# Kernel tuning notes

Measured on AMD Instinct MI355X. Metric: run time of the kernel, lower is better.

The kernel has to match this reference:

```python
import jax, jax.numpy as jnp
import numpy as np

D_EMBED = 512
NUM_HEADS = 8
HEAD_DIM = D_EMBED // NUM_HEADS
D_FF = 2048
B, L = 2, 4096
LN_EPS = 1e-5


def _layernorm(x, g, b):
    mu = jnp.mean(x, axis=-1, keepdims=True)
    var = jnp.mean(jnp.square(x - mu), axis=-1, keepdims=True)
    return (x - mu) * jax.lax.rsqrt(var + LN_EPS) * g + b


def setup_inputs() -> dict:
    key = jax.random.key(0)
    ks = jax.random.split(key, 16)
    s = 0.02
    inp = {
        "x": jax.random.normal(ks[0], (B, L, D_EMBED), dtype=jnp.float32),
        "mask": jnp.ones((B, 1, 1, L), dtype=jnp.int32),
        # attention projections (stored [in, out] for x @ W)
        "Wq": jax.random.normal(ks[1], (D_EMBED, D_EMBED), dtype=jnp.float32) * s,
        "bq": jnp.zeros((D_EMBED,), dtype=jnp.float32),
        "Wk": jax.random.normal(ks[2], (D_EMBED, D_EMBED), dtype=jnp.float32) * s,
        "bk": jnp.zeros((D_EMBED,), dtype=jnp.float32),
        "Wv": jax.random.normal(ks[3], (D_EMBED, D_EMBED), dtype=jnp.float32) * s,
        "bv": jnp.zeros((D_EMBED,), dtype=jnp.float32),
        "Wo": jax.random.normal(ks[4], (D_EMBED, D_EMBED), dtype=jnp.float32) * s,
        "bo": jnp.zeros((D_EMBED,), dtype=jnp.float32),
        # layernorms
        "ln1_g": jnp.ones((D_EMBED,), dtype=jnp.float32),
        "ln1_b": jnp.zeros((D_EMBED,), dtype=jnp.float32),
        "ln2_g": jnp.ones((D_EMBED,), dtype=jnp.float32),
        "ln2_b": jnp.zeros((D_EMBED,), dtype=jnp.float32),
        # FFN
        "W1": jax.random.normal(ks[5], (D_EMBED, D_FF), dtype=jnp.float32) * s,
        "b1": jnp.zeros((D_FF,), dtype=jnp.float32),
        "W2": jax.random.normal(ks[6], (D_FF, D_EMBED), dtype=jnp.float32) * s,
        "b2": jnp.zeros((D_EMBED,), dtype=jnp.float32),
    }
    return inp


def reference(x, mask, Wq, bq, Wk, bk, Wv, bv, Wo, bo, ln1_g, ln1_b,
              W1, b1, W2, b2, ln2_g, ln2_b):
    Bx, Lx, _ = x.shape
    # projections -> [B, H, L, Dh]
    def split_heads(t):
        return t.reshape(Bx, Lx, NUM_HEADS, HEAD_DIM).transpose(0, 2, 1, 3)
    q = split_heads(x @ Wq + bq)
    k = split_heads(x @ Wk + bk)
    v = split_heads(x @ Wv + bv)
    scores = jnp.einsum("bhqd,bhkd->bhqk", q, k) / jnp.sqrt(
        jnp.asarray(HEAD_DIM, dtype=x.dtype))
    scores = jnp.where(mask == 0, jnp.asarray(-1e9, dtype=x.dtype), scores)
    attn = jax.nn.softmax(scores, axis=-1)
    ctx = jnp.einsum("bhqk,bhkd->bhqd", attn, v)
    ctx = ctx.transpose(0, 2, 1, 3).reshape(Bx, Lx, D_EMBED)
    attn_out = ctx @ Wo + bo

    h = _layernorm(x + attn_out, ln1_g, ln1_b)
    ff = (jax.nn.gelu(h @ W1 + b1, approximate=False)) @ W2 + b2
    return _layernorm(h + ff, ln2_g, ln2_b)
```

## Files before the change

kernel.cpp:

```cpp
#include <hip/hip_runtime.h>
#include <hip/hip_bf16.h>
#include <math.h>

#define D_EMBED 512
#define NUM_HEADS 8
#define HEAD_DIM 64
#define D_FF 2048
#define BATCH 2
#define SEQ 4096
#define M_ROWS (BATCH*SEQ)
#define QSCALE 0.18033688011112042f

typedef __attribute__((ext_vector_type(8))) short short8;
typedef __attribute__((ext_vector_type(4))) short short4_t;
typedef __attribute__((ext_vector_type(4))) float f32x4;

#if __has_builtin(__builtin_amdgcn_mfma_f32_16x16x16bf16_1k)
#define MFMA_K16(a,b,c) __builtin_amdgcn_mfma_f32_16x16x16bf16_1k(a,b,c,0,0,0)
#elif __has_builtin(__builtin_amdgcn_mfma_f32_16x16x16_bf16)
#define MFMA_K16(a,b,c) __builtin_amdgcn_mfma_f32_16x16x16_bf16(a,b,c,0,0,0)
#else
#define MFMA_K16(a,b,c) (c)
#endif

#if __has_builtin(__builtin_amdgcn_exp2f)
#define EXP2(x) __builtin_amdgcn_exp2f(x)
#else
#define EXP2(x) exp2f(x)
#endif

__device__ inline unsigned short f2b(float f) {
    union { float f; unsigned u; } v; v.f = f;
    unsigned r = v.u + 0x7fffu + ((v.u >> 16) & 1u);
    return (unsigned short)(r >> 16);
}

__device__ inline float b2f(short s) {
    union { unsigned u; float f; } v;
    v.u = ((unsigned)(unsigned short)s) << 16;
    return v.f;
}

__device__ inline short4_t pk4(float p0, float p1, float p2, float p3) {
    union { __hip_bfloat162 h2[2]; short4_t s4; } u;
    u.h2[0] = __float22bfloat162_rn(make_float2(p0, p1));
    u.h2[1] = __float22bfloat162_rn(make_float2(p2, p3));
    return u.s4;
}

__device__ inline void gl2lds16(const void* g, void* l) {
    __builtin_amdgcn_global_load_lds(
        (const __attribute__((address_space(1))) unsigned int*)g,
        (__attribute__((address_space(3))) unsigned int*)l, 16, 0, 0);
}

template<int EPI>
__global__ __launch_bounds__(256) void gemm_bt(
    const unsigned short* __restrict__ A, const unsigned short* __restrict__ BT,
    const float* __restrict__ bias, void* __restrict__ Cout,
    int M, int N, int K)
{
    __shared__ __align__(16) unsigned short As[128*32];
    __shared__ __align__(16) unsigned short Bs[128*32];
    const int tid  = threadIdx.x;
    const int wave = tid >> 6, lane = tid & 63;
    const int wy = wave >> 1, wx = wave & 1;
    const int quad = lane >> 4, m16 = lane & 15;
    const int row0 = blockIdx.y * 128, n0 = blockIdx.x * 128;
    const int rdoff = (quad ^ ((m16 >> 1) & 3)) * 8;

    f32x4 acc[4][4];
#pragma unroll
    for (int i = 0; i < 4; i++)
#pragma unroll
        for (int j = 0; j < 4; j++) acc[i][j] = (f32x4){0.f,0.f,0.f,0.f};

    const int kIters = K >> 5;
    for (int kt = 0; kt < kIters; ++kt) {
        const int k0 = kt << 5;
#pragma unroll
        for (int it = 0; it < 2; ++it) {
            int g  = it*256 + tid;
            int r  = g >> 2;
            int c8 = (((g & 3) ^ ((g >> 3) & 3)) << 3);
            gl2lds16(A  + (size_t)(row0 + r)*K + k0 + c8, &As[(size_t)(it*256 + wave*64)*8]);
            gl2lds16(BT + (size_t)(n0  + r)*K + k0 + c8, &Bs[(size_t)(it*256 + wave*64)*8]);
        }
        __syncthreads();
        short8 a[4], b[4];
#pragma unroll
        for (int i = 0; i < 4; i++) a[i] = *(const short8*)&As[(wy*64 + i*16 + m16)*32 + rdoff];
#pragma unroll
        for (int j = 0; j < 4; j++) b[j] = *(const short8*)&Bs[(wx*64 + j*16 + m16)*32 + rdoff];
#pragma unroll
        for (int i = 0; i < 4; i++)
#pragma unroll
            for (int j = 0; j < 4; j++)
                acc[i][j] = __builtin_amdgcn_mfma_f32_16x16x32_bf16(a[i], b[j], acc[i][j], 0, 0, 0);
        __syncthreads();
    }

#pragma unroll
    for (int j = 0; j < 4; j++) {
        int col = n0 + wx*64 + j*16 + m16;
        float bj = bias[col];
#pragma unroll
        for (int i = 0; i < 4; i++) {
            int rbase = row0 + wy*64 + i*16 + quad*4;
#pragma unroll
            for (int r = 0; r < 4; r++) {
                float v = acc[i][j][r] + bj;
                size_t idx = (size_t)(rbase + r)*N + col;
                if (EPI == 0) {
                    ((unsigned short*)Cout)[idx] = f2b(v);
                } else {
                    float gv = 0.5f * v * (1.0f + erff(v * 0.70710678118654752f));
                    ((unsigned short*)Cout)[idx] = f2b(gv);
                }
            }
        }
    }
}

__global__ __launch_bounds__(256) void gemm_qkv(
    const unsigned short* __restrict__ A, const unsigned short* __restrict__ BT,
    const float* __restrict__ bias,
    unsigned short* __restrict__ Qp, unsigned short* __restrict__ Kp,
    unsigned short* __restrict__ Vp)
{
    const int K = 512;
    __shared__ __align__(16) unsigned short As[128*32];
    __shared__ __align__(16) unsigned short Bs[128*32];
    const int tid  = threadIdx.x;
    const int wave = tid >> 6, lane = tid & 63;
    const int wy = wave >> 1, wx = wave & 1;
    const int quad = lane >> 4, m16 = lane & 15;
    const int row0 = blockIdx.y * 128, n0 = blockIdx.x * 128;
    const int rdoff = (quad ^ ((m16 >> 1) & 3)) * 8;
    const int region = n0 >> 9;

    f32x4 acc[4][4];
#pragma unroll
    for (int i = 0; i < 4; i++)
#pragma unroll
        for (int j = 0; j < 4; j++) acc[i][j] = (f32x4){0.f,0.f,0.f,0.f};

    for (int kt = 0; kt < 16; ++kt) {
        const int k0 = kt << 5;
#pragma unroll
        for (int it = 0; it < 2; ++it) {
            int g  = it*256 + tid;
            int r  = g >> 2;
            int c8 = (((g & 3) ^ ((g >> 3) & 3)) << 3);
            gl2lds16(A  + (size_t)(row0 + r)*K + k0 + c8, &As[(size_t)(it*256 + wave*64)*8]);
            gl2lds16(BT + (size_t)(n0  + r)*K + k0 + c8, &Bs[(size_t)(it*256 + wave*64)*8]);
        }
        __syncthreads();
        short8 a[4], b[4];
#pragma unroll
        for (int i = 0; i < 4; i++) a[i] = *(const short8*)&As[(wy*64 + i*16 + m16)*32 + rdoff];
#pragma unroll
        for (int j = 0; j < 4; j++) b[j] = *(const short8*)&Bs[(wx*64 + j*16 + m16)*32 + rdoff];
#pragma unroll
        for (int i = 0; i < 4; i++)
#pragma unroll
            for (int j = 0; j < 4; j++)
                acc[i][j] = __builtin_amdgcn_mfma_f32_16x16x32_bf16(a[i], b[j], acc[i][j], 0, 0, 0);
        __syncthreads();
    }

    const float sc = (region == 0) ? QSCALE : 1.0f;
#pragma unroll
    for (int j = 0; j < 4; j++) {
        int col = n0 + wx*64 + j*16 + m16;
        float bj = bias[col];
        int cc = col & 511, h = cc >> 6, d = cc & 63;
#pragma unroll
        for (int i = 0; i < 4; i++) {
            int rbase = row0 + wy*64 + i*16 + quad*4;
#pragma unroll
            for (int r = 0; r < 4; r++) {
                float v = (acc[i][j][r] + bj) * sc;
                int row = rbase + r;
                int b = row >> 12, l = row & 4095;
                size_t bh = (size_t)(b*8 + h);
                if (region == 0) {
                    Qp[(bh*SEQ + l)*64 + d] = f2b(v);
                } else if (region == 1) {
                    Kp[(bh*SEQ + l)*64 + d] = f2b(v);
                } else {
                    int kt = l >> 7, kk = l & 127;
                    int qr = (kk >> 2) & 3, fi = (kk >> 4)*4 + (kk & 3);
                    Vp[((((bh*32 + kt)*4 + qr)*64 + d)*32) + fi] = f2b(v);
                }
            }
        }
    }
}

__global__ __launch_bounds__(256) void gemm_bt64(
    const unsigned short* __restrict__ A, const unsigned short* __restrict__ BT,
    const float* __restrict__ bias, unsigned short* __restrict__ Cout,
    int M, int N, int K)
{
    __shared__ __align__(16) unsigned short As[64*32];
    __shared__ __align__(16) unsigned short Bs[128*32];
    const int tid  = threadIdx.x;
    const int wave = tid >> 6, lane = tid & 63;
    const int wy = wave >> 1, wx = wave & 1;
    const int quad = lane >> 4, m16 = lane & 15;
    const int row0 = blockIdx.y * 64, n0 = blockIdx.x * 128;
    const int rdoff = (quad ^ ((m16 >> 1) & 3)) * 8;

    f32x4 acc[2][4];
#pragma unroll
    for (int i = 0; i < 2; i++)
#pragma unroll
        for (int j = 0; j < 4; j++) acc[i][j] = (f32x4){0.f,0.f,0.f,0.f};

    const int kIters = K >> 5;
    for (int kt = 0; kt < kIters; ++kt) {
        const int k0 = kt << 5;
        {
            int r = tid >> 2;
            int c8 = (((tid & 3) ^ ((tid >> 3) & 3)) << 3);
            gl2lds16(A + (size_t)(row0 + r)*K + k0 + c8, &As[(size_t)(wave*64)*8]);
        }
#pragma unroll
        for (int it = 0; it < 2; ++it) {
            int g  = it*256 + tid;
            int r  = g >> 2;
            int c8 = (((g & 3) ^ ((g >> 3) & 3)) << 3);
            gl2lds16(BT + (size_t)(n0 + r)*K + k0 + c8, &Bs[(size_t)(it*256 + wave*64)*8]);
        }
        __syncthreads();
        short8 a[2], b[4];
#pragma unroll
        for (int i = 0; i < 2; i++) a[i] = *(const short8*)&As[(wy*32 + i*16 + m16)*32 + rdoff];
#pragma unroll
        for (int j = 0; j < 4; j++) b[j] = *(const short8*)&Bs[(wx*64 + j*16 + m16)*32 + rdoff];
#pragma unroll
        for (int i = 0; i < 2; i++)
#pragma unroll
            for (int j = 0; j < 4; j++)
                acc[i][j] = __builtin_amdgcn_mfma_f32_16x16x32_bf16(a[i], b[j], acc[i][j], 0, 0, 0);
        __syncthreads();
    }

#pragma unroll
    for (int j = 0; j < 4; j++) {
        int col = n0 + wx*64 + j*16 + m16;
        float bj = bias[col];
#pragma unroll
        for (int i = 0; i < 2; i++) {
            int rbase = row0 + wy*32 + i*16 + quad*4;
#pragma unroll
            for (int r = 0; r < 4; r++) {
                float v = acc[i][j][r] + bj;
                Cout[(size_t)(rbase + r)*N + col] = f2b(v);
            }
        }
    }
}

__global__ __launch_bounds__(256) void prep(
    const float* __restrict__ Wq, const float* __restrict__ Wk,
    const float* __restrict__ Wv, const float* __restrict__ Wo,
    const float* __restrict__ W1, const float* __restrict__ W2,
    const float* __restrict__ bq, const float* __restrict__ bk,
    const float* __restrict__ bv, const int* __restrict__ mask,
    unsigned short* __restrict__ WqkvT, unsigned short* __restrict__ WoT,
    unsigned short* __restrict__ W1T, unsigned short* __restrict__ W2T,
    float* __restrict__ bqkv, int* __restrict__ mflag, unsigned* __restrict__ kmax2)
{
    const int id = blockIdx.x, t = threadIdx.x;
    if (id == 3072) {
        if (t < 64) {
            const int* m = mask + t*128;
            int all = 1;
            for (int i = 0; i < 128; i += 4) {
                int4 v = *(const int4*)(m + i);
                all &= (v.x && v.y && v.z && v.w) ? 1 : 0;
            }
            mflag[t] = all;
        }
        if (t < 16) kmax2[t] = 0u;
        for (int i = t; i < 1536; i += 256)
            bqkv[i] = (i < 512) ? bq[i] : ((i < 1024) ? bk[i-512] : bv[i-1024]);
        return;
    }
    __shared__ float tt[32][33];
    const float* W; unsigned short* WT; int K, N, bx, by;
    if (id < 256)       { W = Wq; WT = WqkvT;            K = 512;  N = 512;  bx = id & 15;  by = id >> 4; }
    else if (id < 512)  { int l = id - 256;  W = Wk; WT = WqkvT + 512*512;  K = 512;  N = 512;  bx = l & 15; by = l >> 4; }
    else if (id < 768)  { int l = id - 512;  W = Wv; WT = WqkvT + 1024*512; K = 512;  N = 512;  bx = l & 15; by = l >> 4; }
    else if (id < 1024) { int l = id - 768;  W = Wo; WT = WoT;              K = 512;  N = 512;  bx = l & 15; by = l >> 4; }
    else if (id < 2048) { int l = id - 1024; W = W1; WT = W1T;              K = 512;  N = 2048; bx = l & 63; by = l >> 6; }
    else                { int l = id - 2048; W = W2; WT = W2T;              K = 2048; N = 512;  bx = l & 15; by = l >> 4; }
    const int n0 = bx*32, k0 = by*32;
    const int x = t & 31, y = t >> 5;
#pragma unroll
    for (int yy = y; yy < 32; yy += 8) tt[yy][x] = W[(size_t)(k0+yy)*N + n0 + x];
    __syncthreads();
#pragma unroll
    for (int yy = y; yy < 32; yy += 8) WT[(size_t)(n0+yy)*K + k0 + x] = f2b(tt[x][yy]);
}

__global__ __launch_bounds__(256) void kmax_k(
    const unsigned short* __restrict__ Kp, unsigned* __restrict__ kmax2)
{
    const int bh = blockIdx.x, t = threadIdx.x;
    const int row = blockIdx.y*256 + t;
    const unsigned short* kp = Kp + ((size_t)bh*SEQ + row)*64;
    float s = 0.f;
#pragma unroll
    for (int c = 0; c < 8; ++c) {
        short8 v = *(const short8*)(kp + c*8);
#pragma unroll
        for (int j = 0; j < 8; ++j) { float f = b2f(v[j]); s += f*f; }
    }
#pragma unroll
    for (int off = 32; off >= 1; off >>= 1)
        s = fmaxf(s, __shfl_xor(s, off, 64));
    if ((t & 63) == 0) atomicMax(&kmax2[bh], __float_as_uint(s));
}

__global__ __launch_bounds__(256) void flash_attn(
    const unsigned short* __restrict__ Qp, const unsigned short* __restrict__ Kp,
    const unsigned short* __restrict__ Vp, const int* __restrict__ mask,
    const int* __restrict__ flags, const unsigned* __restrict__ kmax2,
    unsigned short* __restrict__ O)
{
    __shared__ __align__(16) unsigned short Ks[2][128*32];
    __shared__ __align__(16) unsigned short Vs[4][64*32];
    const int tid = threadIdx.x, wave = tid >> 6, lane = tid & 63;
    const int quad = lane >> 4, m16 = lane & 15;
    const int bh = blockIdx.y, b = bh >> 3, h = bh & 7;
    const int qbase = blockIdx.x * 64 + wave * 16;
    const int fsw = (m16 >> 1) & 3;
    const int koff = (quad ^ fsw) * 8;

    const unsigned short* Qb = Qp + (size_t)bh*SEQ*64;
    const unsigned short* Kb = Kp + (size_t)bh*SEQ*64;
    const unsigned short* Vb = Vp + (size_t)bh*32*4*64*32;
    const int* mbase = mask + b*SEQ;
    const int* fbase = flags + b*(SEQ/128);

    short8 qf[2];
    {
        const unsigned short* qp = Qb + (size_t)(qbase + m16)*64 + quad*8;
        qf[0] = *(const short8*)qp;
        qf[1] = *(const short8*)(qp + 32);
    }
    float qn2 = 0.f;
#pragma unroll
    for (int j = 0; j < 8; ++j) {
        float f0 = b2f(qf[0][j]), f1 = b2f(qf[1][j]);
        qn2 += f0*f0 + f1*f1;
    }
    qn2 += __shfl_xor(qn2, 16, 64);
    qn2 += __shfl_xor(qn2, 32, 64);
    const float M = sqrtf(qn2 * __uint_as_float(kmax2[bh]));
    const f32x4 cinit = (f32x4){-M, -M, -M, -M};

    f32x4 accO[4];
#pragma unroll
    for (int dj = 0; dj < 4; dj++) accO[dj] = (f32x4){0.f,0.f,0.f,0.f};
    float rs = 0.f;

    for (int kt = 0; kt < SEQ/128; ++kt) {
        const int key0 = kt * 128;
        const int allones = fbase[kt];
        __syncthreads();
#pragma unroll
        for (int it = 0; it < 2; ++it) {
            int g = it*256 + tid;
            int r = g >> 2;
            int c8 = (((g & 3) ^ ((g >> 3) & 3)) << 3);
            gl2lds16(Kb + (size_t)(key0 + r)*64 + c8,      &Ks[0][(it*256 + wave*64)*8]);
            gl2lds16(Kb + (size_t)(key0 + r)*64 + 32 + c8, &Ks[1][(it*256 + wave*64)*8]);
        }
        {
            int d = wave*16 + (lane >> 2), ch = lane & 3;
            int c8 = (ch ^ ((d >> 1) & 3)) * 8;
#pragma unroll
            for (int qr = 0; qr < 4; ++qr)
                gl2lds16(Vb + (((size_t)kt*4 + qr)*64 + d)*32 + c8,
                         &Vs[qr][wave*64*8]);
        }
        __syncthreads();

        short4_t pb[8];
#pragma unroll
        for (int nj = 0; nj < 8; ++nj) {
            short8 k0 = *(const short8*)&Ks[0][(nj*16 + m16)*32 + koff];
            short8 k1 = *(const short8*)&Ks[1][(nj*16 + m16)*32 + koff];
            f32x4 c = cinit;
            c = __builtin_amdgcn_mfma_f32_16x16x32_bf16(k0, qf[0], c, 0, 0, 0);
            c = __builtin_amdgcn_mfma_f32_16x16x32_bf16(k1, qf[1], c, 0, 0, 0);
            if (!allones) {
                int4 mv = *(const int4*)(mbase + key0 + nj*16 + quad*4);
                c[0] = mv.x ? c[0] : -1e9f;
                c[1] = mv.y ? c[1] : -1e9f;
                c[2] = mv.z ? c[2] : -1e9f;
                c[3] = mv.w ? c[3] : -1e9f;
            }
            float p0 = EXP2(c[0]);
            float p1 = EXP2(c[1]);
            float p2 = EXP2(c[2]);
            float p3 = EXP2(c[3]);
            rs += (p0 + p1) + (p2 + p3);
            pb[nj] = pk4(p0, p1, p2, p3);
        }

#pragma unroll
        for (int l = 0; l < 4; ++l) {
#pragma unroll
            for (int dj = 0; dj < 4; ++dj) {
                const unsigned short* vrow = &Vs[quad][(dj*16 + m16)*32 + ((l ^ fsw) * 8)];
                short4_t vlo = *(const short4_t*)vrow;
                short4_t vhi = *(const short4_t*)(vrow + 4);
                accO[dj] = MFMA_K16(vlo, pb[2*l],     accO[dj]);
                accO[dj] = MFMA_K16(vhi, pb[2*l + 1], accO[dj]);
            }
        }
    }

    rs += __shfl_xor(rs, 16, 64);
    rs += __shfl_xor(rs, 32, 64);
    float rl = 1.0f / rs;
#pragma unroll
    for (int dj = 0; dj < 4; ++dj) {
        short4_t o = pk4(accO[dj][0]*rl, accO[dj][1]*rl,
                         accO[dj][2]*rl, accO[dj][3]*rl);
        *(short4_t*)&O[(size_t)(b*SEQ + qbase + m16)*D_EMBED
                       + h*HEAD_DIM + dj*16 + quad*4] = o;
    }
}

__global__ __launch_bounds__(256) void ln_res1(
    const float* __restrict__ A, const unsigned short* __restrict__ Bv,
    const float* __restrict__ g, const float* __restrict__ be,
    unsigned short* __restrict__ Yb)
{
    const int wave = threadIdx.x >> 6, lane = threadIdx.x & 63;
    const int row = blockIdx.x * 4 + wave;
    const float* ap = A + (size_t)row*512 + lane*8;
    short8 bv = *(const short8*)(Bv + (size_t)row*512 + lane*8);
    float v[8]; float s = 0.f;
#pragma unroll
    for (int j = 0; j < 8; j++) { v[j] = ap[j] + b2f(bv[j]); s += v[j]; }
#pragma unroll
    for (int off = 32; off >= 1; off >>= 1) s += __shfl_xor(s, off, 64);
    float mu = s * (1.f/512.f);
    float q = 0.f;
#pragma unroll
    for (int j = 0; j < 8; j++) { v[j] -= mu; q += v[j]*v[j]; }
#pragma unroll
    for (int off = 32; off >= 1; off >>= 1) q += __shfl_xor(q, off, 64);
    float rstd = rsqrtf(q * (1.f/512.f) + 1e-5f);
#pragma unroll
    for (int j = 0; j < 8; j++) {
        float y = v[j]*rstd*g[lane*8+j] + be[lane*8+j];
        Yb[(size_t)row*512 + lane*8 + j] = f2b(y);
    }
}

__global__ __launch_bounds__(256) void ln_res2(
    const unsigned short* __restrict__ A, const unsigned short* __restrict__ Bv,
    const float* __restrict__ g, const float* __restrict__ be,
    float* __restrict__ Yf)
{
    const int wave = threadIdx.x >> 6, lane = threadIdx.x & 63;
    const int row = blockIdx.x * 4 + wave;
    short8 av = *(const short8*)(A  + (size_t)row*512 + lane*8);
    short8 bv = *(const short8*)(Bv + (size_t)row*512 + lane*8);
    float v[8]; float s = 0.f;
#pragma unroll
    for (int j = 0; j < 8; j++) { v[j] = b2f(av[j]) + b2f(bv[j]); s += v[j]; }
#pragma unroll
    for (int off = 32; off >= 1; off >>= 1) s += __shfl_xor(s, off, 64);
    float mu = s * (1.f/512.f);
    float q = 0.f;
#pragma unroll
    for (int j = 0; j < 8; j++) { v[j] -= mu; q += v[j]*v[j]; }
#pragma unroll
    for (int off = 32; off >= 1; off >>= 1) q += __shfl_xor(q, off, 64);
    float rstd = rsqrtf(q * (1.f/512.f) + 1e-5f);
#pragma unroll
    for (int j = 0; j < 8; j++) {
        float y = v[j]*rstd*g[lane*8+j] + be[lane*8+j];
        Yf[(size_t)row*512 + lane*8 + j] = y;
    }
}

__global__ __launch_bounds__(256) void cvt_f32_bf16(
    const float* __restrict__ X, unsigned short* __restrict__ Y, int n)
{
    int idx = (blockIdx.x * 256 + threadIdx.x) * 4;
    if (idx < n) {
        float4 v = *(const float4*)(X + idx);
        Y[idx+0] = f2b(v.x); Y[idx+1] = f2b(v.y);
        Y[idx+2] = f2b(v.z); Y[idx+3] = f2b(v.w);
    }
}

extern "C" void kernel_launch(void* const* d_in, const int* in_sizes, int n_in,
                              void* d_out, int out_size, void* d_ws, size_t ws_size,
                              hipStream_t stream)
{
    const float* x    = (const float*)d_in[0];
    const int*   mask = (const int*)  d_in[1];
    const float* Wq = (const float*)d_in[2];  const float* bq = (const float*)d_in[3];
    const float* Wk = (const float*)d_in[4];  const float* bk = (const float*)d_in[5];
    const float* Wv = (const float*)d_in[6];  const float* bv = (const float*)d_in[7];
    const float* Wo = (const float*)d_in[8];  const float* bo = (const float*)d_in[9];
    const float* ln1g = (const float*)d_in[10]; const float* ln1b = (const float*)d_in[11];
    const float* ln2g = (const float*)d_in[12]; const float* ln2b = (const float*)d_in[13];
    const float* W1 = (const float*)d_in[14]; const float* b1 = (const float*)d_in[15];
    const float* W2 = (const float*)d_in[16]; const float* b2 = (const float*)d_in[17];
    float* out = (float*)d_out;

    char* ws = (char*)d_ws;
    const size_t MB = 1024*1024;
    unsigned short* xb    = (unsigned short*)(ws + 0);
    unsigned short* WqkvT = (unsigned short*)(ws + 8*MB);
    unsigned short* W1T   = (unsigned short*)(ws + 10*MB);
    unsigned short* W2T   = (unsigned short*)(ws + 12*MB);
    unsigned short* WoT   = (unsigned short*)(ws + 14*MB);
    float*          bqkv  = (float*)(ws + 14*MB + 512*1024);
    int*            mflag = (int*)(ws + 14*MB + 768*1024);
    unsigned*       kmaxb = (unsigned*)(ws + 14*MB + 772*1024);
    unsigned short* Qp    = (unsigned short*)(ws + 15*MB);
    unsigned short* Kp    = (unsigned short*)(ws + 23*MB);
    unsigned short* Vp    = (unsigned short*)(ws + 31*MB);
    unsigned short* ctx   = (unsigned short*)(ws + 39*MB);
    unsigned short* atfb  = (unsigned short*)(ws + 47*MB);
    unsigned short* hb    = (unsigned short*)(ws + 0);
    unsigned short* Gb    = (unsigned short*)(ws + 15*MB);
    unsigned short* ffb   = (unsigned short*)(ws + 47*MB);

    cvt_f32_bf16<<<4096, 256, 0, stream>>>(x, xb, M_ROWS*D_EMBED);
    prep<<<3073, 256, 0, stream>>>(Wq, Wk, Wv, Wo, W1, W2, bq, bk, bv, mask,
                                   WqkvT, WoT, W1T, W2T, bqkv, mflag, kmaxb);

    gemm_qkv<<<dim3(12,64), 256, 0, stream>>>(xb, WqkvT, bqkv, Qp, Kp, Vp);

    kmax_k<<<dim3(16,16), 256, 0, stream>>>(Kp, kmaxb);
    flash_attn<<<dim3(SEQ/64, 16), 256, 0, stream>>>(Qp, Kp, Vp, mask, mflag, kmaxb, ctx);

    gemm_bt64<<<dim3(4,128), 256, 0, stream>>>(ctx, WoT, bo, atfb, M_ROWS, 512, 512);
    ln_res1<<<M_ROWS/4, 256, 0, stream>>>(x, atfb, ln1g, ln1b, hb);

    gemm_bt<2><<<dim3(16,64), 256, 0, stream>>>(hb, W1T, b1, Gb, M_ROWS, D_FF, 512);
    gemm_bt64<<<dim3(4,128), 256, 0, stream>>>(Gb, W2T, b2, ffb, M_ROWS, 512, D_FF);
    ln_res2<<<M_ROWS/4, 256, 0, stream>>>(hb, ffb, ln2g, ln2b, out);
}
```

Baseline: 377.1 us.

## Rewrite flash attention with 32x32 MFMA, 64 queries per wave, double-buffered K/V

The attention kernel now handles 64 queries per wave (256 per block) using 32x32x16 bf16 MFMA tiles, so each K/V tile loaded into LDS is reused across four times as many queries. K and V tiles for the next 128-key step are prefetched into a second LDS buffer while the current one is computed, which removes one barrier per iteration. V is now stored transposed as [bh][d][seq], and the P fragments are rearranged in registers with permlane32 swaps. The cost is a grid of only 256 blocks with a heavier register footprint, which can hurt occupancy and leave some CUs underused.

```diff
diff --git a/kernel.cpp b/kernel.cpp
--- a/kernel.cpp
+++ b/kernel.cpp
@@ -14,14 +14,7 @@
 typedef __attribute__((ext_vector_type(8))) short short8;
 typedef __attribute__((ext_vector_type(4))) short short4_t;
 typedef __attribute__((ext_vector_type(4))) float f32x4;
-
-#if __has_builtin(__builtin_amdgcn_mfma_f32_16x16x16bf16_1k)
-#define MFMA_K16(a,b,c) __builtin_amdgcn_mfma_f32_16x16x16bf16_1k(a,b,c,0,0,0)
-#elif __has_builtin(__builtin_amdgcn_mfma_f32_16x16x16_bf16)
-#define MFMA_K16(a,b,c) __builtin_amdgcn_mfma_f32_16x16x16_bf16(a,b,c,0,0,0)
-#else
-#define MFMA_K16(a,b,c) (c)
-#endif
+typedef __attribute__((ext_vector_type(16))) float f32x16;
 
 #if __has_builtin(__builtin_amdgcn_exp2f)
 #define EXP2(x) __builtin_amdgcn_exp2f(x)
@@ -46,6 +39,36 @@
     u.h2[0] = __float22bfloat162_rn(make_float2(p0, p1));
     u.h2[1] = __float22bfloat162_rn(make_float2(p2, p3));
     return u.s4;
+}
+
+__device__ inline unsigned pk2(float lo, float hi) {
+    union { __hip_bfloat162 h2; unsigned u; } x;
+    x.h2 = __float22bfloat162_rn(make_float2(lo, hi));
+    return x.u;
+}
+
+__device__ inline void plswap(unsigned a, unsigned b, unsigned &r0, unsigned &r1) {
+#if __has_builtin(__builtin_amdgcn_permlane32_swap)
+    auto v = __builtin_amdgcn_permlane32_swap(a, b, false, false);
+    r0 = (unsigned)v[0]; r1 = (unsigned)v[1];
+#else
+    unsigned ax = (unsigned)__shfl_xor((int)a, 32, 64);
+    unsigned bx = (unsigned)__shfl_xor((int)b, 32, 64);
+    bool hi = (threadIdx.x & 32) != 0;
+    r0 = hi ? bx : a;
+    r1 = hi ? b  : ax;
+#endif
+}
+
+__device__ inline short8 pfrag8(const float* p) {
+    unsigned a0 = pk2(p[0], p[1]), a1 = pk2(p[2], p[3]);
+    unsigned b0 = pk2(p[4], p[5]), b1 = pk2(p[6], p[7]);
+    unsigned u0, u1, u2, u3;
+    plswap(a0, b0, u0, u1);
+    plswap(a1, b1, u2, u3);
+    union { unsigned u[4]; short8 s; } r;
+    r.u[0] = u0; r.u[1] = u2; r.u[2] = u1; r.u[3] = u3;
+    return r.s;
 }
 
 __device__ inline void gl2lds16(const void* g, void* l) {
@@ -189,9 +212,7 @@
                 } else if (region == 1) {
                     Kp[(bh*SEQ + l)*64 + d] = f2b(v);
                 } else {
-                    int kt = l >> 7, kk = l & 127;
-                    int qr = (kk >> 2) & 3, fi = (kk >> 4)*4 + (kk & 3);
-                    Vp[((((bh*32 + kt)*4 + qr)*64 + d)*32) + fi] = f2b(v);
+                    Vp[(bh*64 + d)*SEQ + l] = f2b(v);
                 }
             }
         }
@@ -325,116 +346,151 @@
     if ((t & 63) == 0) atomicMax(&kmax2[bh], __float_as_uint(s));
 }
 
-__global__ __launch_bounds__(256) void flash_attn(
+__global__ __launch_bounds__(256, 1) void flash_attn(
     const unsigned short* __restrict__ Qp, const unsigned short* __restrict__ Kp,
-    const unsigned short* __restrict__ Vp, const int* __restrict__ mask,
+    const unsigned short* __restrict__ Vt, const int* __restrict__ mask,
     const int* __restrict__ flags, const unsigned* __restrict__ kmax2,
     unsigned short* __restrict__ O)
 {
-    __shared__ __align__(16) unsigned short Ks[2][128*32];
-    __shared__ __align__(16) unsigned short Vs[4][64*32];
+    __shared__ __align__(16) unsigned short Ks[2][128*64];
+    __shared__ __align__(16) unsigned short Vs[2][64*128];
     const int tid = threadIdx.x, wave = tid >> 6, lane = tid & 63;
-    const int quad = lane >> 4, m16 = lane & 15;
+    const int c = lane & 31, l5 = lane >> 5;
     const int bh = blockIdx.y, b = bh >> 3, h = bh & 7;
-    const int qbase = blockIdx.x * 64 + wave * 16;
-    const int fsw = (m16 >> 1) & 3;
-    const int koff = (quad ^ fsw) * 8;
+    const int qbase = blockIdx.x * 256 + wave * 64;
 
     const unsigned short* Qb = Qp + (size_t)bh*SEQ*64;
     const unsigned short* Kb = Kp + (size_t)bh*SEQ*64;
-    const unsigned short* Vb = Vp + (size_t)bh*32*4*64*32;
+    const unsigned short* Vb = Vt + (size_t)bh*64*SEQ;
     const int* mbase = mask + b*SEQ;
     const int* fbase = flags + b*(SEQ/128);
-
-    short8 qf[2];
-    {
-        const unsigned short* qp = Qb + (size_t)(qbase + m16)*64 + quad*8;
-        qf[0] = *(const short8*)qp;
-        qf[1] = *(const short8*)(qp + 32);
-    }
-    float qn2 = 0.f;
-#pragma unroll
-    for (int j = 0; j < 8; ++j) {
-        float f0 = b2f(qf[0][j]), f1 = b2f(qf[1][j]);
-        qn2 += f0*f0 + f1*f1;
-    }
-    qn2 += __shfl_xor(qn2, 16, 64);
-    qn2 += __shfl_xor(qn2, 32, 64);
-    const float M = sqrtf(qn2 * __uint_as_float(kmax2[bh]));
-    const f32x4 cinit = (f32x4){-M, -M, -M, -M};
-
-    f32x4 accO[4];
-#pragma unroll
-    for (int dj = 0; dj < 4; dj++) accO[dj] = (f32x4){0.f,0.f,0.f,0.f};
-    float rs = 0.f;
+    const float kmx = __uint_as_float(kmax2[bh]);
+
+    short8 qf[2][4];
+    float Mq[2];
+#pragma unroll
+    for (int qs = 0; qs < 2; ++qs) {
+        const unsigned short* qp = Qb + (size_t)(qbase + qs*32 + c)*64 + l5*8;
+        float qn2 = 0.f;
+#pragma unroll
+        for (int t = 0; t < 4; ++t) {
+            qf[qs][t] = *(const short8*)(qp + t*16);
+#pragma unroll
+            for (int j = 0; j < 8; ++j) { float f = b2f(qf[qs][t][j]); qn2 += f*f; }
+        }
+        qn2 += __shfl_xor(qn2, 32, 64);
+        Mq[qs] = sqrtf(qn2 * kmx);
+    }
+
+    f32x16 accO[2][2];
+#pragma unroll
+    for (int qs = 0; qs < 2; ++qs)
+#pragma unroll
+        for (int dg = 0; dg < 2; ++dg)
+#pragma unroll
+            for (int r = 0; r < 16; ++r) accO[qs][dg][r] = 0.f;
+    float rs0 = 0.f, rs1 = 0.f;
+
+#define STAGE(nb, ktn) do {                                                   \
+        const int key0s = (ktn)*128;                                          \
+        _Pragma("unroll")                                                     \
+        for (int it = 0; it < 4; ++it) {                                      \
+            int idx = it*256 + tid;                                           \
+            int r = idx >> 3, chn = idx & 7;                                  \
+            gl2lds16(Kb + (size_t)(key0s + r)*64 + ((chn ^ (r & 7)) << 3),    \
+                     &Ks[nb][(it*256 + wave*64)*8]);                          \
+        }                                                                     \
+        _Pragma("unroll")                                                     \
+        for (int it = 0; it < 4; ++it) {                                      \
+            int idx = it*256 + tid;                                           \
+            int r = idx >> 4, chn = idx & 15;                                 \
+            gl2lds16(Vb + (size_t)r*SEQ + key0s + ((chn ^ (r & 15)) << 3),    \
+                     &Vs[nb][(it*256 + wave*64)*8]);                          \
+        }                                                                     \
+    } while (0)
+
+    STAGE(0, 0);
+    __syncthreads();
+    int cb = 0;
 
     for (int kt = 0; kt < SEQ/128; ++kt) {
+        if (kt + 1 < SEQ/128) STAGE(cb ^ 1, kt + 1);
+        const int allones = fbase[kt];
         const int key0 = kt * 128;
-        const int allones = fbase[kt];
+        const unsigned short* Kt  = Ks[cb];
+        const unsigned short* Vtl = Vs[cb];
+
+#pragma unroll
+        for (int kg = 0; kg < 4; ++kg) {
+            short8 kf[4];
+#pragma unroll
+            for (int t = 0; t < 4; ++t) {
+                int row = kg*32 + c;
+                int chn = (t*2 + l5) ^ (row & 7);
+                kf[t] = *(const short8*)&Kt[row*64 + chn*8];
+            }
+            f32x16 s0, s1;
+#pragma unroll
+            for (int r = 0; r < 16; ++r) { s0[r] = -Mq[0]; s1[r] = -Mq[1]; }
+#pragma unroll
+            for (int t = 0; t < 4; ++t) {
+                s0 = __builtin_amdgcn_mfma_f32_32x32x16_bf16(kf[t], qf[0][t], s0, 0, 0, 0);
+                s1 = __builtin_amdgcn_mfma_f32_32x32x16_bf16(kf[t], qf[1][t], s1, 0, 0, 0);
+            }
+            if (!allones) {
+#pragma unroll
+                for (int r = 0; r < 16; ++r) {
+                    int mv = mbase[key0 + kg*32 + (r & 3) + 8*(r >> 2) + 4*l5];
+                    if (!mv) { s0[r] = -1e9f; s1[r] = -1e9f; }
+                }
+            }
+            float pa[16], pc[16];
+#pragma unroll
+            for (int r = 0; r < 16; ++r) { pa[r] = EXP2(s0[r]); pc[r] = EXP2(s1[r]); }
+            rs0 += (((pa[0]+pa[1])+(pa[2]+pa[3])) + ((pa[4]+pa[5])+(pa[6]+pa[7])))
+                 + (((pa[8]+pa[9])+(pa[10]+pa[11])) + ((pa[12]+pa[13])+(pa[14]+pa[15])));
+            rs1 += (((pc[0]+pc[1])+(pc[2]+pc[3])) + ((pc[4]+pc[5])+(pc[6]+pc[7])))
+                 + (((pc[8]+pc[9])+(pc[10]+pc[11])) + ((pc[12]+pc[13])+(pc[14]+pc[15])));
+
+            short8 vf[2][2];
+#pragma unroll
+            for (int c2 = 0; c2 < 2; ++c2)
+#pragma unroll
+                for (int dg = 0; dg < 2; ++dg) {
+                    int row = dg*32 + c;
+                    int chn = ((kg*2 + c2)*2 + l5) ^ (row & 15);
+                    vf[c2][dg] = *(const short8*)&Vtl[row*128 + chn*8];
+                }
+#pragma unroll
+            for (int c2 = 0; c2 < 2; ++c2) {
+                short8 pf0 = pfrag8(&pa[c2*8]);
+                short8 pf1 = pfrag8(&pc[c2*8]);
+                accO[0][0] = __builtin_amdgcn_mfma_f32_32x32x16_bf16(vf[c2][0], pf0, accO[0][0], 0, 0, 0);
+                accO[0][1] = __builtin_amdgcn_mfma_f32_32x32x16_bf16(vf[c2][1], pf0, accO[0][1], 0, 0, 0);
+                accO[1][0] = __builtin_amdgcn_mfma_f32_32x32x16_bf16(vf[c2][0], pf1, accO[1][0], 0, 0, 0);
+                accO[1][1] = __builtin_amdgcn_mfma_f32_32x32x16_bf16(vf[c2][1], pf1, accO[1][1], 0, 0, 0);
+            }
+        }
         __syncthreads();
-#pragma unroll
-        for (int it = 0; it < 2; ++it) {
-            int g = it*256 + tid;
-            int r = g >> 2;
-            int c8 = (((g & 3) ^ ((g >> 3) & 3)) << 3);
-            gl2lds16(Kb + (size_t)(key0 + r)*64 + c8,      &Ks[0][(it*256 + wave*64)*8]);
-            gl2lds16(Kb + (size_t)(key0 + r)*64 + 32 + c8, &Ks[1][(it*256 + wave*64)*8]);
-        }
-        {
-            int d = wave*16 + (lane >> 2), ch = lane & 3;
-            int c8 = (ch ^ ((d >> 1) & 3)) * 8;
-#pragma unroll
-            for (int qr = 0; qr < 4; ++qr)
-                gl2lds16(Vb + (((size_t)kt*4 + qr)*64 + d)*32 + c8,
-                         &Vs[qr][wave*64*8]);
-        }
-        __syncthreads();
-
-        short4_t pb[8];
-#pragma unroll
-        for (int nj = 0; nj < 8; ++nj) {
-            short8 k0 = *(const short8*)&Ks[0][(nj*16 + m16)*32 + koff];
-            short8 k1 = *(const short8*)&Ks[1][(nj*16 + m16)*32 + koff];
-            f32x4 c = cinit;
-            c = __builtin_amdgcn_mfma_f32_16x16x32_bf16(k0, qf[0], c, 0, 0, 0);
-            c = __builtin_amdgcn_mfma_f32_16x16x32_bf16(k1, qf[1], c, 0, 0, 0);
-            if (!allones) {
-                int4 mv = *(const int4*)(mbase + key0 + nj*16 + quad*4);
-                c[0] = mv.x ? c[0] : -1e9f;
-                c[1] = mv.y ? c[1] : -1e9f;
-                c[2] = mv.z ? c[2] : -1e9f;
-                c[3] = mv.w ? c[3] : -1e9f;
-            }
-            float p0 = EXP2(c[0]);
-            float p1 = EXP2(c[1]);
-            float p2 = EXP2(c[2]);
-            float p3 = EXP2(c[3]);
-            rs += (p0 + p1) + (p2 + p3);
-            pb[nj] = pk4(p0, p1, p2, p3);
-        }
-
-#pragma unroll
-        for (int l = 0; l < 4; ++l) {
-#pragma unroll
-            for (int dj = 0; dj < 4; ++dj) {
-                const unsigned short* vrow = &Vs[quad][(dj*16 + m16)*32 + ((l ^ fsw) * 8)];
-                short4_t vlo = *(const short4_t*)vrow;
-                short4_t vhi = *(const short4_t*)(vrow + 4);
-                accO[dj] = MFMA_K16(vlo, pb[2*l],     accO[dj]);
-                accO[dj] = MFMA_K16(vhi, pb[2*l + 1], accO[dj]);
-            }
-        }
-    }
-
-    rs += __shfl_xor(rs, 16, 64);
-    rs += __shfl_xor(rs, 32, 64);
-    float rl = 1.0f / rs;
-#pragma unroll
-    for (int dj = 0; dj < 4; ++dj) {
-        short4_t o = pk4(accO[dj][0]*rl, accO[dj][1]*rl,
-                         accO[dj][2]*rl, accO[dj][3]*rl);
-        *(short4_t*)&O[(size_t)(b*SEQ + qbase + m16)*D_EMBED
-                       + h*HEAD_DIM + dj*16 + quad*4] = o;
+        cb ^= 1;
+    }
+#undef STAGE
+
+    rs0 += __shfl_xor(rs0, 32, 64);
+    rs1 += __shfl_xor(rs1, 32, 64);
+    float rl[2] = { 1.0f/rs0, 1.0f/rs1 };
+#pragma unroll
+    for (int qs = 0; qs < 2; ++qs) {
+        int qrow = qbase + qs*32 + c;
+        unsigned short* op = O + (size_t)(b*SEQ + qrow)*D_EMBED + h*HEAD_DIM;
+#pragma unroll
+        for (int dg = 0; dg < 2; ++dg)
+#pragma unroll
+            for (int q4 = 0; q4 < 4; ++q4) {
+                short4_t o = pk4(accO[qs][dg][q4*4+0]*rl[qs], accO[qs][dg][q4*4+1]*rl[qs],
+                                 accO[qs][dg][q4*4+2]*rl[qs], accO[qs][dg][q4*4+3]*rl[qs]);
+                *(short4_t*)&op[dg*32 + q4*8 + l5*4] = o;
+            }
     }
 }
 
@@ -547,7 +603,7 @@
     gemm_qkv<<<dim3(12,64), 256, 0, stream>>>(xb, WqkvT, bqkv, Qp, Kp, Vp);
 
     kmax_k<<<dim3(16,16), 256, 0, stream>>>(Kp, kmaxb);
-    flash_attn<<<dim3(SEQ/64, 16), 256, 0, stream>>>(Qp, Kp, Vp, mask, mflag, kmaxb, ctx);
+    flash_attn<<<dim3(SEQ/256, 16), 256, 0, stream>>>(Qp, Kp, Vp, mask, mflag, kmaxb, ctx);
 
     gemm_bt64<<<dim3(4,128), 256, 0, stream>>>(ctx, WoT, bo, atfb, M_ROWS, 512, 512);
     ln_res1<<<M_ROWS/4, 256, 0, stream>>>(x, atfb, ln1g, ln1b, hb);
```

New measurement: 373.7 us. No clear change (-0.9%).
